# Kernel optimization log

Measured on AMD Instinct MI355X. Metric: run time of the kernel, lower is better.

Reference implementation:

```python
import jax, jax.numpy as jnp
import numpy as np

B, S, H, E, V, NSTEPS = 8, 128, 512, 512, 32000, 8


def setup_inputs() -> dict:
    key = jax.random.key(0)
    ks = jax.random.split(key, 24)

    def lin(k, fi, fo):
        return (jax.random.normal(k, (fi, fo), jnp.float32) / np.sqrt(fi).astype(np.float32))

    return {
        "input_ids": jax.random.randint(ks[0], (B, S), 0, V),
        "tree_ids": jax.random.randint(ks[1], (B, NSTEPS, 3, S), 0, S),
        "emb": jax.random.normal(ks[2], (V, E), jnp.float32) * 0.02,
        "W_ioux": lin(ks[3], E, 3 * H),
        "W_iouh_r": lin(ks[4], H, 3 * H),
        "b_iouh_r": jnp.zeros((3 * H,), jnp.float32),
        "W_iouh_l": lin(ks[5], H, 3 * H),
        "b_iouh_l": jnp.zeros((3 * H,), jnp.float32),
        "W_fx": lin(ks[6], E, H),
        "W_fh0": lin(ks[7], H, H),
        "b_fh0": jnp.zeros((H,), jnp.float32),
        "W_fh1": lin(ks[8], H, H),
        "b_fh1": jnp.zeros((H,), jnp.float32),
        "W_fh2": lin(ks[9], H, H),
        "b_fh2": jnp.zeros((H,), jnp.float32),
        "W_fh3": lin(ks[10], H, H),
        "b_fh3": jnp.zeros((H,), jnp.float32),
    }


def _scatter_rows(vals, idx):
    # out[b, idx[b, j], k] += vals[b, j, k]  (torch scatter_add_ along dim 1)
    return jax.vmap(lambda v, i: jnp.zeros_like(v).at[i].add(v))(vals, idx)


def _gather_rows(vals, idx):
    # out[b, j, k] = vals[b, idx[b, j], k]  (torch gather along dim 1)
    return jnp.take_along_axis(vals, idx[:, :, None], axis=1)


def _masked_scatter(dest, mask_rows, src):
    # Exact torch masked_scatter_ semantics: flatten mask/src, fill True slots
    # with consecutive elements of flattened src.
    m = jnp.broadcast_to(mask_rows[:, :, None], dest.shape).reshape(-1)
    pos = jnp.clip(jnp.cumsum(m) - 1, 0, None)
    out = jnp.where(m, src.reshape(-1)[pos], dest.reshape(-1))
    return out.reshape(dest.shape)


def reference(input_ids, tree_ids, emb, W_ioux, W_iouh_r, b_iouh_r, W_iouh_l,
              b_iouh_l, W_fx, W_fh0, b_fh0, W_fh1, b_fh1, W_fh2, b_fh2,
              W_fh3, b_fh3):
    x = emb[input_ids]                      # [B, S, E]
    Hs = W_fx.shape[1]
    iou_x = x @ W_ioux                      # [B, S, 3H], loop-invariant
    fx_x = x @ W_fx                         # [B, S, H],  loop-invariant
    h0 = jnp.zeros(x.shape[:2] + (Hs,), x.dtype)
    c0 = jnp.zeros_like(h0)
    steps = jnp.transpose(tree_ids, (1, 0, 2, 3))  # [n_steps, B, 3, S]

    def step(carry, t):
        h, c = carry
        idx_d, idx_r, idx_l = t[:, 0], t[:, 1], t[:, 2]
        iou_hr = h @ W_iouh_r + b_iouh_r
        iou_hl = h @ W_iouh_l + b_iouh_l
        # torch scatter_add_ with an index of width H into a 3H buffer only
        # touches the first H channels -- replicate that exactly.
        scat = _scatter_rows(iou_hr[..., :Hs], idx_r) + _scatter_rows(iou_hl[..., :Hs], idx_l)
        iou = iou_x.at[..., :Hs].add(scat)
        i, o, u = jnp.split(iou, 3, axis=-1)
        i, o, u = jax.nn.sigmoid(i), jax.nn.sigmoid(o), jnp.tanh(u)
        # fh0 and fh1 share idx_r, fh2 and fh3 share idx_l -> fold linearly.
        fh_r = h @ (W_fh0 + W_fh1) + (b_fh0 + b_fh1)
        fh_l = h @ (W_fh2 + W_fh3) + (b_fh2 + b_fh3)
        f = jax.nn.sigmoid(_gather_rows(fx_x, idx_d)
                           + _gather_rows(fh_r, idx_r)
                           + _gather_rows(fh_l, idx_l))
        fc = f * c
        c_full = i * u + _scatter_rows(fc, idx_d)
        h_full = o * jnp.tanh(c_full)
        mask = idx_d != 0
        h_new = _masked_scatter(h, mask, h_full)
        c_new = _masked_scatter(c, mask, c_full)
        return (h_new, c_new), None

    (h, c), _ = jax.lax.scan(step, (h0, c0), steps)
    return h
```

## Files before the change

kernel.cpp:

```cpp
#include <hip/hip_runtime.h>
#include <hip/hip_bf16.h>

#define B_ 8
#define S_ 128
#define H_ 512
#define E_ 512
#define NST 8
#define R_ 1024
#define N2 2048
#define KD 512
#define LDA 72
#define TM 64
#define TN 64

typedef __hip_bfloat16 bf16;
typedef __attribute__((ext_vector_type(8))) short v8s;
typedef __attribute__((ext_vector_type(4))) float v4f;

__device__ __forceinline__ float sigm(float x){ return 1.0f/(1.0f + expf(-x)); }
__device__ __forceinline__ float load_in(const void* p, long long i, int isb){
    return isb ? __bfloat162float(((const bf16*)p)[i]) : ((const float*)p)[i];
}
__device__ __forceinline__ int idx_read(const int* p, int j, int is64){
    return is64 ? p[2*j] : p[j];
}
__device__ __forceinline__ unsigned short f2b(float v){
    bf16 b = __float2bfloat16(v);
    return *(unsigned short*)&b;
}

__global__ void probe_all(const void* t0, const void* t1, const void* t2, const void* t3,
                          const void* t4, const void* t5, const void* t6, const void* t7,
                          const void* t8, const void* t9, const void* t10, const void* t11,
                          const void* t12, const void* t13, const void* t14,
                          const int* __restrict__ ids, const int* __restrict__ tree,
                          int* __restrict__ flags){
    const void* ts[15] = {t0,t1,t2,t3,t4,t5,t6,t7,t8,t9,t10,t11,t12,t13,t14};
    int bid = blockIdx.x, t = threadIdx.x;
    int bad = 0;
    if (bid < 15){
        if (t < 512){
            unsigned short u = ((const unsigned short*)ts[bid])[t];
            bad = (((u >> 7) & 0xFF) >= 140);
        }
    } else {
        const int* p = (bid == 15) ? ids : tree;
        int n = (bid == 15) ? 1024 : 2048;
        for (int j = t; j < n; j += 1024)
            if (j & 1) bad |= (p[j] != 0);
    }
    unsigned long long bl = __ballot(bad);
    __shared__ int acc[16];
    if ((t & 63) == 0) acc[t >> 6] = (bl != 0ull) ? 1 : 0;
    __syncthreads();
    if (t == 0){
        int any = 0;
        for (int w = 0; w < 16; ++w) any |= acc[w];
        flags[(bid < 15) ? bid : (16 + bid - 15)] = (bid < 15) ? (any ? 0 : 1) : (any ? 0 : 1);
    }
}

__global__ void rank_count(const int* __restrict__ tree, int* __restrict__ msk,
                           int* __restrict__ rnk, int* __restrict__ cnt,
                           const int* __restrict__ flags){
    int is64 = flags[17];
    int st = blockIdx.x;
    int t  = threadIdx.x;
    cnt[(0*NST + st)*R_ + t] = 0;
    cnt[(1*NST + st)*R_ + t] = 0;
    cnt[(2*NST + st)*R_ + t] = 0;
    __syncthreads();
    int b = t >> 7, s = t & 127;
    int base = (b*NST + st)*3*S_;
    int d0 = idx_read(tree, base + s, is64);
    int rd = (b<<7) + d0;
    int rr = (b<<7) + idx_read(tree, base + S_ + s, is64);
    int rl = (b<<7) + idx_read(tree, base + 2*S_ + s, is64);
    int m = (d0 != 0) ? 1 : 0;
    unsigned long long bal = __ballot(m);
    int lane = t & 63, wave = t >> 6;
    __shared__ int wtot[16];
    if (lane == 0) wtot[wave] = __popcll(bal);
    __syncthreads();
    int bp = 0;
    for (int w = 0; w < wave; ++w) bp += wtot[w];
    int rank = bp + __popcll(bal & ((1ull << lane) - 1ull));
    msk[st*R_ + t] = m;
    rnk[st*R_ + t] = m ? rank : 0;
    atomicAdd(&cnt[(0*NST + st)*R_ + rr], 1);
    atomicAdd(&cnt[(1*NST + st)*R_ + rl], 1);
    atomicAdd(&cnt[(2*NST + st)*R_ + rd], 1);
}

__global__ void csr_scan(const int* __restrict__ cnt, int* __restrict__ off,
                         int* __restrict__ cur){
    int st = blockIdx.x, a = blockIdx.y;
    int t = threadIdx.x;
    int base = (a*NST + st)*R_;
    __shared__ int sh[R_];
    int v = cnt[base + t];
    sh[t] = v;
    __syncthreads();
    for (int d = 1; d < R_; d <<= 1){
        int x = (t >= d) ? sh[t - d] : 0;
        __syncthreads();
        sh[t] += x;
        __syncthreads();
    }
    int excl = sh[t] - v;
    off[base + t] = excl;
    cur[base + t] = excl;
}

__global__ void csr_fill(const int* __restrict__ tree, int* __restrict__ cur,
                         int* __restrict__ ent, const int* __restrict__ flags){
    int is64 = flags[17];
    int st = blockIdx.x;
    int t = threadIdx.x;
    int b = t >> 7, s = t & 127;
    int base = (b*NST + st)*3*S_;
    int rd = (b<<7) + idx_read(tree, base + s, is64);
    int rr = (b<<7) + idx_read(tree, base + S_ + s, is64);
    int rl = (b<<7) + idx_read(tree, base + 2*S_ + s, is64);
    int p0 = atomicAdd(&cur[(0*NST + st)*R_ + rr], 1);
    ent[(0*NST + st)*R_ + p0] = t;
    int p1 = atomicAdd(&cur[(1*NST + st)*R_ + rl], 1);
    ent[(1*NST + st)*R_ + p1] = t;
    int p2 = atomicAdd(&cur[(2*NST + st)*R_ + rd], 1);
    ent[(2*NST + st)*R_ + p2] = t | (rr << 10) | (rl << 20);
}

__global__ __launch_bounds__(256)
void pack_all(const void* __restrict__ Wioux, const void* __restrict__ Wfx,
              const void* __restrict__ Wr, const void* __restrict__ Wl,
              const void* __restrict__ W0, const void* __restrict__ W1,
              const void* __restrict__ W2, const void* __restrict__ W3,
              const void* __restrict__ br, const void* __restrict__ bl,
              const void* __restrict__ b0, const void* __restrict__ b1,
              const void* __restrict__ b2, const void* __restrict__ b3,
              const int* __restrict__ ids, const void* __restrict__ emb,
              unsigned short* __restrict__ WxT, unsigned short* __restrict__ WcatT,
              float* __restrict__ bcat, unsigned short* __restrict__ xb,
              float* __restrict__ h0, unsigned short* __restrict__ hb,
              const int* __restrict__ flags){
    int bid = blockIdx.x, tid = threadIdx.x;
    if (bid < 512){
        int f_wx = flags[1], f_wf = flags[6];
        int n = (bid & 7)*256 + tid;
        int k0 = (bid >> 3)*8;
        unsigned short tmp[8];
        #pragma unroll
        for (int i = 0; i < 8; ++i){
            float v = (n < 1536) ? load_in(Wioux, (long long)(k0+i)*1536 + n, f_wx)
                                 : load_in(Wfx,   (long long)(k0+i)*512 + (n-1536), f_wf);
            tmp[i] = f2b(v);
        }
        *(v8s*)&WxT[(size_t)n*KD + k0] = *(v8s*)tmp;
    } else if (bid < 1024){
        int fWr=flags[2], fWl=flags[4], fW0=flags[7], fW1=flags[9], fW2=flags[11], fW3=flags[13];
        int bb = bid - 512;
        int n = (bb & 7)*256 + tid;
        int k0 = (bb >> 3)*8;
        unsigned short tmp[8];
        #pragma unroll
        for (int i = 0; i < 8; ++i){
            long long k = k0 + i;
            float v;
            if      (n <  512) v = load_in(Wr, k*1536 + n, fWr);
            else if (n < 1024) v = load_in(Wl, k*1536 + (n-512), fWl);
            else if (n < 1536) { int c = n-1024; v = load_in(W0, k*512+c, fW0) + load_in(W1, k*512+c, fW1); }
            else               { int c = n-1536; v = load_in(W2, k*512+c, fW2) + load_in(W3, k*512+c, fW3); }
            tmp[i] = f2b(v);
        }
        *(v8s*)&WcatT[(size_t)n*KD + k0] = *(v8s*)tmp;
    } else if (bid < 1032){
        int fbr=flags[3], fbl=flags[5], fb0=flags[8], fb1=flags[10], fb2=flags[12], fb3=flags[14];
        int n = (bid - 1024)*256 + tid;
        float v;
        if      (n <  512) v = load_in(br, n, fbr);
        else if (n < 1024) v = load_in(bl, n-512, fbl);
        else if (n < 1536) v = load_in(b0, n-1024, fb0) + load_in(b1, n-1024, fb1);
        else               v = load_in(b2, n-1536, fb2) + load_in(b3, n-1536, fb3);
        bcat[n] = v;
    } else if (bid < 1288){
        int f_emb = flags[0], i64 = flags[16];
        int id = (bid - 1032)*256 + tid;
        int r = id >> 6, c0 = (id & 63)*8;
        long long base = (long long)idx_read(ids, r, i64)*E_ + c0;
        unsigned short tmp[8];
        #pragma unroll
        for (int i = 0; i < 8; ++i) tmp[i] = f2b(load_in(emb, base + i, f_emb));
        *(v8s*)&xb[(size_t)r*KD + c0] = *(v8s*)tmp;
    } else if (bid < 2312){
        int idx = (bid - 1288)*256 + tid;
        ((float4*)h0)[idx] = make_float4(0.f, 0.f, 0.f, 0.f);
    } else {
        int idx = (bid - 2312)*256 + tid;
        ((float4*)hb)[idx] = make_float4(0.f, 0.f, 0.f, 0.f);
    }
}

__global__ __launch_bounds__(256)
void gemm_bf16(const unsigned short* __restrict__ A,
               const unsigned short* __restrict__ BT,
               const float* __restrict__ bias,
               float* __restrict__ C){
    __shared__ short As[TM*LDA];
    __shared__ short Bs[TN*LDA];
    int bn = blockIdx.x, bm = blockIdx.y;
    int tid = threadIdx.x;
    int lane = tid & 63, wave = tid >> 6;
    int wm = wave & 1, wn = wave >> 1;
    int lm = lane & 15, quad = lane >> 4;
    v4f acc[2][2];
    #pragma unroll
    for (int i=0;i<2;++i)
        #pragma unroll
        for (int j=0;j<2;++j) acc[i][j] = (v4f)0.0f;

    int srow = tid >> 3, sg = (tid & 7)*8;
    const unsigned short* Ab = A  + (size_t)(bm*TM)*KD;
    const unsigned short* Bb = BT + (size_t)(bn*TN)*KD;
    v8s pa[2], pb[2];
    #pragma unroll
    for (int j=0;j<2;++j){
        pa[j] = *(const v8s*)(Ab + (size_t)(j*32+srow)*KD + sg);
        pb[j] = *(const v8s*)(Bb + (size_t)(j*32+srow)*KD + sg);
    }
    for (int k0 = 0; k0 < KD; k0 += 64){
        #pragma unroll
        for (int j=0;j<2;++j){
            *(v8s*)&As[(j*32+srow)*LDA + sg] = pa[j];
            *(v8s*)&Bs[(j*32+srow)*LDA + sg] = pb[j];
        }
        __syncthreads();
        int k1 = k0 + 64;
        if (k1 < KD){
            #pragma unroll
            for (int j=0;j<2;++j){
                pa[j] = *(const v8s*)(Ab + (size_t)(j*32+srow)*KD + k1 + sg);
                pb[j] = *(const v8s*)(Bb + (size_t)(j*32+srow)*KD + k1 + sg);
            }
        }
        #pragma unroll
        for (int kk = 0; kk < 64; kk += 32){
            v8s af[2], bf[2];
            #pragma unroll
            for (int i=0;i<2;++i){
                af[i] = *(const v8s*)&As[(wm*32 + i*16 + lm)*LDA + kk + quad*8];
                bf[i] = *(const v8s*)&Bs[(wn*32 + i*16 + lm)*LDA + kk + quad*8];
            }
            #pragma unroll
            for (int i=0;i<2;++i)
                #pragma unroll
                for (int j=0;j<2;++j)
                    acc[i][j] = __builtin_amdgcn_mfma_f32_16x16x32_bf16(af[i], bf[j], acc[i][j], 0, 0, 0);
        }
        __syncthreads();
    }
    #pragma unroll
    for (int j=0;j<2;++j){
        int n = bn*TN + wn*32 + j*16 + lm;
        float bv = bias ? bias[n] : 0.0f;
        #pragma unroll
        for (int i=0;i<2;++i){
            int m0 = bm*TM + wm*32 + i*16 + quad*4;
            #pragma unroll
            for (int rg = 0; rg < 4; ++rg)
                C[(size_t)(m0+rg)*N2 + n] = acc[i][j][rg] + bv;
        }
    }
}

__global__ __launch_bounds__(256)
void step_fused(const float* __restrict__ XO, const float* __restrict__ T,
                const float* __restrict__ h_old, const float* __restrict__ c_old,
                float* __restrict__ h_new, float* __restrict__ c_new,
                unsigned short* __restrict__ hb,
                const int* __restrict__ msk, const int* __restrict__ rnk,
                const int* __restrict__ cnt, const int* __restrict__ off,
                const int* __restrict__ ent, int st){
    int r = blockIdx.x;
    if (!msk[st*R_ + r]){
        for (int c = threadIdx.x; c < H_; c += 256){
            float hv = h_old[(size_t)r*H_ + c];
            h_new[(size_t)r*H_ + c] = hv;
            c_new[(size_t)r*H_ + c] = c_old[(size_t)r*H_ + c];
            hb[(size_t)r*KD + c] = f2b(hv);
        }
        return;
    }
    int j = rnk[st*R_ + r];
    int bR = off[(0*NST + st)*R_ + j], dR = cnt[(0*NST + st)*R_ + j];
    int bL = off[(1*NST + st)*R_ + j], dL = cnt[(1*NST + st)*R_ + j];
    int bD = off[(2*NST + st)*R_ + j], dD = cnt[(2*NST + st)*R_ + j];
    const int* eR = ent + (0*NST + st)*R_ + bR;
    const int* eL = ent + (1*NST + st)*R_ + bL;
    const int* eD = ent + (2*NST + st)*R_ + bD;
    const float* xo = XO + (size_t)j*N2;
    for (int c = threadIdx.x; c < H_; c += 256){
        float scat = 0.f;
        for (int e = 0; e < dR; ++e) scat += T[(size_t)eR[e]*N2 + c];
        for (int e = 0; e < dL; ++e) scat += T[(size_t)eL[e]*N2 + 512 + c];
        float fxv = xo[1536 + c];
        float csc = 0.f;
        for (int e = 0; e < dD; ++e){
            int pk = eD[e];
            int s  = pk & 1023, rr = (pk >> 10) & 1023, rl = (pk >> 20) & 1023;
            float f = sigm(fxv + T[(size_t)rr*N2 + 1024 + c] + T[(size_t)rl*N2 + 1536 + c]);
            csc += f * c_old[(size_t)s*H_ + c];
        }
        float ig = sigm(xo[c] + scat);
        float og = sigm(xo[512 + c]);
        float ug = tanhf(xo[1024 + c]);
        float cf = ig*ug + csc;
        float hf = og * tanhf(cf);
        h_new[(size_t)r*H_ + c] = hf;
        c_new[(size_t)r*H_ + c] = cf;
        hb[(size_t)r*KD + c] = f2b(hf);
    }
}

extern "C" void kernel_launch(void* const* d_in, const int* in_sizes, int n_in,
                              void* d_out, int out_size, void* d_ws, size_t ws_size,
                              hipStream_t stream) {
    const int* input_ids = (const int*)d_in[0];
    const int* tree      = (const int*)d_in[1];

    char* p = (char*)d_ws;
    auto alloc = [&](size_t bytes) -> void* {
        void* q = (void*)p;
        p += (bytes + 255) & ~(size_t)255;
        return q;
    };
    float*          XO     = (float*)alloc((size_t)R_*N2*4);
    float*          T      = (float*)alloc((size_t)R_*N2*4);
    float*          h0     = (float*)alloc((size_t)R_*H_*4);
    float*          c0     = (float*)alloc((size_t)R_*H_*4);
    float*          h1     = (float*)alloc((size_t)R_*H_*4);
    float*          c1     = (float*)alloc((size_t)R_*H_*4);
    unsigned short* WxT    = (unsigned short*)alloc((size_t)N2*KD*2);
    unsigned short* WcatT  = (unsigned short*)alloc((size_t)N2*KD*2);
    float*          bcat   = (float*)alloc((size_t)N2*4);
    unsigned short* xb     = (unsigned short*)alloc((size_t)R_*KD*2);
    unsigned short* hb     = (unsigned short*)alloc((size_t)R_*KD*2);
    int*            msk    = (int*)alloc((size_t)NST*R_*4);
    int*            rnk    = (int*)alloc((size_t)NST*R_*4);
    int*            cnt    = (int*)alloc((size_t)3*NST*R_*4);
    int*            off    = (int*)alloc((size_t)3*NST*R_*4);
    int*            cur    = (int*)alloc((size_t)3*NST*R_*4);
    int*            ent    = (int*)alloc((size_t)3*NST*R_*4);
    int*            flags  = (int*)alloc(256);

    hipLaunchKernelGGL(probe_all, dim3(17), dim3(1024), 0, stream,
                       d_in[2], d_in[3], d_in[4], d_in[5], d_in[6], d_in[7], d_in[8],
                       d_in[9], d_in[10], d_in[11], d_in[12], d_in[13], d_in[14],
                       d_in[15], d_in[16], input_ids, tree, flags);
    hipLaunchKernelGGL(rank_count, dim3(NST), dim3(R_), 0, stream, tree, msk, rnk, cnt, flags);
    hipLaunchKernelGGL(csr_scan, dim3(NST, 3), dim3(R_), 0, stream, cnt, off, cur);
    hipLaunchKernelGGL(csr_fill, dim3(NST), dim3(R_), 0, stream, tree, cur, ent, flags);
    hipLaunchKernelGGL(pack_all, dim3(2568), dim3(256), 0, stream,
                       d_in[3], d_in[8],
                       d_in[4], d_in[6], d_in[9], d_in[11], d_in[13], d_in[15],
                       d_in[5], d_in[7], d_in[10], d_in[12], d_in[14], d_in[16],
                       input_ids, d_in[2],
                       WxT, WcatT, bcat, xb, h0, hb, flags);

    hipLaunchKernelGGL(gemm_bf16, dim3(N2/TN, R_/TM), dim3(256), 0, stream,
                       xb, WxT, (const float*)nullptr, XO);

    float *hc = h0, *cc = c0, *hn = h1, *cn = c1;
    for (int st = 0; st < NST; ++st){
        hipLaunchKernelGGL(gemm_bf16, dim3(N2/TN, R_/TM), dim3(256), 0, stream,
                           hb, WcatT, bcat, T);
        hipLaunchKernelGGL(step_fused, dim3(R_), dim3(256), 0, stream,
                           XO, T, hc, cc, hn, cn, hb, msk, rnk, cnt, off, ent, st);
        float* th = hc; hc = hn; hn = th;
        float* tc = cc; cc = cn; cn = tc;
    }
    hipMemcpyAsync(d_out, hc, (size_t)R_*H_*4, hipMemcpyDeviceToDevice, stream);
}
```

Baseline: 324.8 us.

## Merge setup kernels, peel first step GEMM, write final step directly to output

Fuses the rank/count setup into the weight-packing kernel so fewer launches are needed, and uses a grid-stride pack with 512-thread blocks. The first recurrence step skips its GEMM, since h is zero and the projection reduces to the bias; it reads bcat with stride 0. The last step writes straight into the output buffer, dropping the final device-to-device copy. The step epilogue uses one thread per channel with 512-thread blocks. Zero-initialisation of hb is removed because step 0 now writes every row.

```diff
diff --git a/kernel.cpp b/kernel.cpp
--- a/kernel.cpp
+++ b/kernel.cpp
@@ -10,8 +10,6 @@
 #define N2 2048
 #define KD 512
 #define LDA 72
-#define TM 64
-#define TN 64
 
 typedef __hip_bfloat16 bf16;
 typedef __attribute__((ext_vector_type(8))) short v8s;
@@ -56,40 +54,122 @@
     if (t == 0){
         int any = 0;
         for (int w = 0; w < 16; ++w) any |= acc[w];
-        flags[(bid < 15) ? bid : (16 + bid - 15)] = (bid < 15) ? (any ? 0 : 1) : (any ? 0 : 1);
-    }
-}
-
-__global__ void rank_count(const int* __restrict__ tree, int* __restrict__ msk,
-                           int* __restrict__ rnk, int* __restrict__ cnt,
-                           const int* __restrict__ flags){
+        flags[(bid < 15) ? bid : (16 + bid - 15)] = any ? 0 : 1;
+    }
+}
+
+#define NB2 320
+#define GS2 (NB2*512)
+__global__ __launch_bounds__(512)
+void rank_pack(const void* __restrict__ Wioux, const void* __restrict__ Wfx,
+               const void* __restrict__ Wr, const void* __restrict__ Wl,
+               const void* __restrict__ W0, const void* __restrict__ W1,
+               const void* __restrict__ W2, const void* __restrict__ W3,
+               const void* __restrict__ br, const void* __restrict__ bl,
+               const void* __restrict__ b0, const void* __restrict__ b1,
+               const void* __restrict__ b2, const void* __restrict__ b3,
+               const int* __restrict__ ids, const void* __restrict__ emb,
+               const int* __restrict__ tree,
+               unsigned short* __restrict__ WxT, unsigned short* __restrict__ WcatT,
+               float* __restrict__ bcat, unsigned short* __restrict__ xb,
+               float* __restrict__ h0,
+               int* __restrict__ msk, int* __restrict__ rnk, int* __restrict__ cnt,
+               const int* __restrict__ flags){
+    int bid = blockIdx.x, tid = threadIdx.x;
     int is64 = flags[17];
-    int st = blockIdx.x;
-    int t  = threadIdx.x;
-    cnt[(0*NST + st)*R_ + t] = 0;
-    cnt[(1*NST + st)*R_ + t] = 0;
-    cnt[(2*NST + st)*R_ + t] = 0;
-    __syncthreads();
-    int b = t >> 7, s = t & 127;
-    int base = (b*NST + st)*3*S_;
-    int d0 = idx_read(tree, base + s, is64);
-    int rd = (b<<7) + d0;
-    int rr = (b<<7) + idx_read(tree, base + S_ + s, is64);
-    int rl = (b<<7) + idx_read(tree, base + 2*S_ + s, is64);
-    int m = (d0 != 0) ? 1 : 0;
-    unsigned long long bal = __ballot(m);
-    int lane = t & 63, wave = t >> 6;
-    __shared__ int wtot[16];
-    if (lane == 0) wtot[wave] = __popcll(bal);
-    __syncthreads();
-    int bp = 0;
-    for (int w = 0; w < wave; ++w) bp += wtot[w];
-    int rank = bp + __popcll(bal & ((1ull << lane) - 1ull));
-    msk[st*R_ + t] = m;
-    rnk[st*R_ + t] = m ? rank : 0;
-    atomicAdd(&cnt[(0*NST + st)*R_ + rr], 1);
-    atomicAdd(&cnt[(1*NST + st)*R_ + rl], 1);
-    atomicAdd(&cnt[(2*NST + st)*R_ + rd], 1);
+    if (bid < 8){
+        int st = bid;
+        for (int c = tid; c < R_; c += 512){
+            cnt[(0*NST + st)*R_ + c] = 0;
+            cnt[(1*NST + st)*R_ + c] = 0;
+            cnt[(2*NST + st)*R_ + c] = 0;
+        }
+        __syncthreads();
+        __shared__ int wt[8];
+        int runbase = 0;
+        for (int ch = 0; ch < 2; ++ch){
+            int t = ch*512 + tid;
+            int b = t >> 7, s = t & 127;
+            int base = (b*NST + st)*3*S_;
+            int d0 = idx_read(tree, base + s, is64);
+            int rd = (b<<7) + d0;
+            int rr = (b<<7) + idx_read(tree, base + S_ + s, is64);
+            int rl = (b<<7) + idx_read(tree, base + 2*S_ + s, is64);
+            int m = (d0 != 0) ? 1 : 0;
+            unsigned long long bal = __ballot(m);
+            int lane = tid & 63, wv = tid >> 6;
+            if (lane == 0) wt[wv] = __popcll(bal);
+            __syncthreads();
+            int bp = runbase, tot = 0;
+            for (int w = 0; w < wv; ++w) bp += wt[w];
+            for (int w = 0; w < 8; ++w) tot += wt[w];
+            int rank = bp + __popcll(bal & ((1ull << lane) - 1ull));
+            msk[st*R_ + t] = m;
+            rnk[st*R_ + t] = m ? rank : 0;
+            atomicAdd(&cnt[(0*NST + st)*R_ + rr], 1);
+            atomicAdd(&cnt[(1*NST + st)*R_ + rl], 1);
+            atomicAdd(&cnt[(2*NST + st)*R_ + rd], 1);
+            runbase += tot;
+            __syncthreads();
+        }
+    }
+    int gt = bid*512 + tid;
+    {
+        int f_wx = flags[1], f_wf = flags[6];
+        for (int u = gt; u < 131072; u += GS2){
+            int n = u >> 6, k0 = (u & 63)*8;
+            unsigned short tmp[8];
+            #pragma unroll
+            for (int i = 0; i < 8; ++i){
+                float v = (n < 1536) ? load_in(Wioux, (long long)(k0+i)*1536 + n, f_wx)
+                                     : load_in(Wfx,   (long long)(k0+i)*512 + (n-1536), f_wf);
+                tmp[i] = f2b(v);
+            }
+            *(v8s*)&WxT[(size_t)n*KD + k0] = *(v8s*)tmp;
+        }
+    }
+    {
+        int fWr=flags[2], fWl=flags[4], fW0=flags[7], fW1=flags[9], fW2=flags[11], fW3=flags[13];
+        for (int u = gt; u < 131072; u += GS2){
+            int n = u >> 6, k0 = (u & 63)*8;
+            unsigned short tmp[8];
+            #pragma unroll
+            for (int i = 0; i < 8; ++i){
+                long long k = k0 + i;
+                float v;
+                if      (n <  512) v = load_in(Wr, k*1536 + n, fWr);
+                else if (n < 1024) v = load_in(Wl, k*1536 + (n-512), fWl);
+                else if (n < 1536) { int c = n-1024; v = load_in(W0, k*512+c, fW0) + load_in(W1, k*512+c, fW1); }
+                else               { int c = n-1536; v = load_in(W2, k*512+c, fW2) + load_in(W3, k*512+c, fW3); }
+                tmp[i] = f2b(v);
+            }
+            *(v8s*)&WcatT[(size_t)n*KD + k0] = *(v8s*)tmp;
+        }
+    }
+    {
+        int fbr=flags[3], fbl=flags[5], fb0=flags[8], fb1=flags[10], fb2=flags[12], fb3=flags[14];
+        for (int n = gt; n < 2048; n += GS2){
+            float v;
+            if      (n <  512) v = load_in(br, n, fbr);
+            else if (n < 1024) v = load_in(bl, n-512, fbl);
+            else if (n < 1536) v = load_in(b0, n-1024, fb0) + load_in(b1, n-1024, fb1);
+            else               v = load_in(b2, n-1536, fb2) + load_in(b3, n-1536, fb3);
+            bcat[n] = v;
+        }
+    }
+    {
+        int f_emb = flags[0], i64i = flags[16];
+        for (int u = gt; u < 65536; u += GS2){
+            int r = u >> 6, c0 = (u & 63)*8;
+            long long base = (long long)idx_read(ids, r, i64i)*E_ + c0;
+            unsigned short tmp[8];
+            #pragma unroll
+            for (int i = 0; i < 8; ++i) tmp[i] = f2b(load_in(emb, base + i, f_emb));
+            *(v8s*)&xb[(size_t)r*KD + c0] = *(v8s*)tmp;
+        }
+    }
+    for (int u = gt; u < 262144; u += GS2)
+        ((float4*)h0)[u] = make_float4(0.f,0.f,0.f,0.f);
 }
 
 __global__ void csr_scan(const int* __restrict__ cnt, int* __restrict__ off,
@@ -112,91 +192,24 @@
     cur[base + t] = excl;
 }
 
-__global__ void csr_fill(const int* __restrict__ tree, int* __restrict__ cur,
-                         int* __restrict__ ent, const int* __restrict__ flags){
+__global__ __launch_bounds__(512)
+void csr_fill(const int* __restrict__ tree, int* __restrict__ cur,
+              int* __restrict__ ent, const int* __restrict__ flags){
     int is64 = flags[17];
     int st = blockIdx.x;
-    int t = threadIdx.x;
-    int b = t >> 7, s = t & 127;
-    int base = (b*NST + st)*3*S_;
-    int rd = (b<<7) + idx_read(tree, base + s, is64);
-    int rr = (b<<7) + idx_read(tree, base + S_ + s, is64);
-    int rl = (b<<7) + idx_read(tree, base + 2*S_ + s, is64);
-    int p0 = atomicAdd(&cur[(0*NST + st)*R_ + rr], 1);
-    ent[(0*NST + st)*R_ + p0] = t;
-    int p1 = atomicAdd(&cur[(1*NST + st)*R_ + rl], 1);
-    ent[(1*NST + st)*R_ + p1] = t;
-    int p2 = atomicAdd(&cur[(2*NST + st)*R_ + rd], 1);
-    ent[(2*NST + st)*R_ + p2] = t | (rr << 10) | (rl << 20);
-}
-
-__global__ __launch_bounds__(256)
-void pack_all(const void* __restrict__ Wioux, const void* __restrict__ Wfx,
-              const void* __restrict__ Wr, const void* __restrict__ Wl,
-              const void* __restrict__ W0, const void* __restrict__ W1,
-              const void* __restrict__ W2, const void* __restrict__ W3,
-              const void* __restrict__ br, const void* __restrict__ bl,
-              const void* __restrict__ b0, const void* __restrict__ b1,
-              const void* __restrict__ b2, const void* __restrict__ b3,
-              const int* __restrict__ ids, const void* __restrict__ emb,
-              unsigned short* __restrict__ WxT, unsigned short* __restrict__ WcatT,
-              float* __restrict__ bcat, unsigned short* __restrict__ xb,
-              float* __restrict__ h0, unsigned short* __restrict__ hb,
-              const int* __restrict__ flags){
-    int bid = blockIdx.x, tid = threadIdx.x;
-    if (bid < 512){
-        int f_wx = flags[1], f_wf = flags[6];
-        int n = (bid & 7)*256 + tid;
-        int k0 = (bid >> 3)*8;
-        unsigned short tmp[8];
-        #pragma unroll
-        for (int i = 0; i < 8; ++i){
-            float v = (n < 1536) ? load_in(Wioux, (long long)(k0+i)*1536 + n, f_wx)
-                                 : load_in(Wfx,   (long long)(k0+i)*512 + (n-1536), f_wf);
-            tmp[i] = f2b(v);
-        }
-        *(v8s*)&WxT[(size_t)n*KD + k0] = *(v8s*)tmp;
-    } else if (bid < 1024){
-        int fWr=flags[2], fWl=flags[4], fW0=flags[7], fW1=flags[9], fW2=flags[11], fW3=flags[13];
-        int bb = bid - 512;
-        int n = (bb & 7)*256 + tid;
-        int k0 = (bb >> 3)*8;
-        unsigned short tmp[8];
-        #pragma unroll
-        for (int i = 0; i < 8; ++i){
-            long long k = k0 + i;
-            float v;
-            if      (n <  512) v = load_in(Wr, k*1536 + n, fWr);
-            else if (n < 1024) v = load_in(Wl, k*1536 + (n-512), fWl);
-            else if (n < 1536) { int c = n-1024; v = load_in(W0, k*512+c, fW0) + load_in(W1, k*512+c, fW1); }
-            else               { int c = n-1536; v = load_in(W2, k*512+c, fW2) + load_in(W3, k*512+c, fW3); }
-            tmp[i] = f2b(v);
-        }
-        *(v8s*)&WcatT[(size_t)n*KD + k0] = *(v8s*)tmp;
-    } else if (bid < 1032){
-        int fbr=flags[3], fbl=flags[5], fb0=flags[8], fb1=flags[10], fb2=flags[12], fb3=flags[14];
-        int n = (bid - 1024)*256 + tid;
-        float v;
-        if      (n <  512) v = load_in(br, n, fbr);
-        else if (n < 1024) v = load_in(bl, n-512, fbl);
-        else if (n < 1536) v = load_in(b0, n-1024, fb0) + load_in(b1, n-1024, fb1);
-        else               v = load_in(b2, n-1536, fb2) + load_in(b3, n-1536, fb3);
-        bcat[n] = v;
-    } else if (bid < 1288){
-        int f_emb = flags[0], i64 = flags[16];
-        int id = (bid - 1032)*256 + tid;
-        int r = id >> 6, c0 = (id & 63)*8;
-        long long base = (long long)idx_read(ids, r, i64)*E_ + c0;
-        unsigned short tmp[8];
-        #pragma unroll
-        for (int i = 0; i < 8; ++i) tmp[i] = f2b(load_in(emb, base + i, f_emb));
-        *(v8s*)&xb[(size_t)r*KD + c0] = *(v8s*)tmp;
-    } else if (bid < 2312){
-        int idx = (bid - 1288)*256 + tid;
-        ((float4*)h0)[idx] = make_float4(0.f, 0.f, 0.f, 0.f);
-    } else {
-        int idx = (bid - 2312)*256 + tid;
-        ((float4*)hb)[idx] = make_float4(0.f, 0.f, 0.f, 0.f);
+    for (int ch = 0; ch < 2; ++ch){
+        int t = ch*512 + threadIdx.x;
+        int b = t >> 7, s = t & 127;
+        int base = (b*NST + st)*3*S_;
+        int rd = (b<<7) + idx_read(tree, base + s, is64);
+        int rr = (b<<7) + idx_read(tree, base + S_ + s, is64);
+        int rl = (b<<7) + idx_read(tree, base + 2*S_ + s, is64);
+        int p0 = atomicAdd(&cur[(0*NST + st)*R_ + rr], 1);
+        ent[(0*NST + st)*R_ + p0] = t;
+        int p1 = atomicAdd(&cur[(1*NST + st)*R_ + rl], 1);
+        ent[(1*NST + st)*R_ + p1] = t;
+        int p2 = atomicAdd(&cur[(2*NST + st)*R_ + rd], 1);
+        ent[(2*NST + st)*R_ + p2] = t | (rr << 10) | (rl << 20);
     }
 }
 
@@ -205,8 +218,8 @@
                const unsigned short* __restrict__ BT,
                const float* __restrict__ bias,
                float* __restrict__ C){
-    __shared__ short As[TM*LDA];
-    __shared__ short Bs[TN*LDA];
+    __shared__ short As[64*LDA];
+    __shared__ short Bs[64*LDA];
     int bn = blockIdx.x, bm = blockIdx.y;
     int tid = threadIdx.x;
     int lane = tid & 63, wave = tid >> 6;
@@ -219,8 +232,8 @@
         for (int j=0;j<2;++j) acc[i][j] = (v4f)0.0f;
 
     int srow = tid >> 3, sg = (tid & 7)*8;
-    const unsigned short* Ab = A  + (size_t)(bm*TM)*KD;
-    const unsigned short* Bb = BT + (size_t)(bn*TN)*KD;
+    const unsigned short* Ab = A  + (size_t)(bm*64)*KD;
+    const unsigned short* Bb = BT + (size_t)(bn*64)*KD;
     v8s pa[2], pb[2];
     #pragma unroll
     for (int j=0;j<2;++j){
@@ -260,11 +273,11 @@
     }
     #pragma unroll
     for (int j=0;j<2;++j){
-        int n = bn*TN + wn*32 + j*16 + lm;
+        int n = bn*64 + wn*32 + j*16 + lm;
         float bv = bias ? bias[n] : 0.0f;
         #pragma unroll
         for (int i=0;i<2;++i){
-            int m0 = bm*TM + wm*32 + i*16 + quad*4;
+            int m0 = bm*64 + wm*32 + i*16 + quad*4;
             #pragma unroll
             for (int rg = 0; rg < 4; ++rg)
                 C[(size_t)(m0+rg)*N2 + n] = acc[i][j][rg] + bv;
@@ -272,53 +285,51 @@
     }
 }
 
-__global__ __launch_bounds__(256)
-void step_fused(const float* __restrict__ XO, const float* __restrict__ T,
-                const float* __restrict__ h_old, const float* __restrict__ c_old,
-                float* __restrict__ h_new, float* __restrict__ c_new,
-                unsigned short* __restrict__ hb,
-                const int* __restrict__ msk, const int* __restrict__ rnk,
-                const int* __restrict__ cnt, const int* __restrict__ off,
-                const int* __restrict__ ent, int st){
-    int r = blockIdx.x;
+__global__ __launch_bounds__(512)
+void step_epi(const float* __restrict__ XO, const float* __restrict__ T, int tstr,
+              const float* __restrict__ hc, const float* __restrict__ cc,
+              float* __restrict__ hn, float* __restrict__ cn,
+              unsigned short* __restrict__ hb, float* __restrict__ out,
+              const int* __restrict__ msk, const int* __restrict__ rnk,
+              const int* __restrict__ cnt, const int* __restrict__ off,
+              const int* __restrict__ ent, int st, int last){
+    int r = blockIdx.x, c = threadIdx.x;
     if (!msk[st*R_ + r]){
-        for (int c = threadIdx.x; c < H_; c += 256){
-            float hv = h_old[(size_t)r*H_ + c];
-            h_new[(size_t)r*H_ + c] = hv;
-            c_new[(size_t)r*H_ + c] = c_old[(size_t)r*H_ + c];
-            hb[(size_t)r*KD + c] = f2b(hv);
-        }
+        float hv = hc[(size_t)r*H_ + c];
+        if (last){ out[(size_t)r*H_ + c] = hv; return; }
+        hn[(size_t)r*H_ + c] = hv;
+        cn[(size_t)r*H_ + c] = cc[(size_t)r*H_ + c];
+        hb[(size_t)r*KD + c] = f2b(hv);
         return;
     }
     int j = rnk[st*R_ + r];
-    int bR = off[(0*NST + st)*R_ + j], dR = cnt[(0*NST + st)*R_ + j];
-    int bL = off[(1*NST + st)*R_ + j], dL = cnt[(1*NST + st)*R_ + j];
-    int bD = off[(2*NST + st)*R_ + j], dD = cnt[(2*NST + st)*R_ + j];
-    const int* eR = ent + (0*NST + st)*R_ + bR;
-    const int* eL = ent + (1*NST + st)*R_ + bL;
-    const int* eD = ent + (2*NST + st)*R_ + bD;
+    int bR = off[(0*NST+st)*R_ + j], dR = cnt[(0*NST+st)*R_ + j];
+    int bL = off[(1*NST+st)*R_ + j], dL = cnt[(1*NST+st)*R_ + j];
+    int bD = off[(2*NST+st)*R_ + j], dD = cnt[(2*NST+st)*R_ + j];
+    const int* eR = ent + (0*NST+st)*R_ + bR;
+    const int* eL = ent + (1*NST+st)*R_ + bL;
+    const int* eD = ent + (2*NST+st)*R_ + bD;
     const float* xo = XO + (size_t)j*N2;
-    for (int c = threadIdx.x; c < H_; c += 256){
-        float scat = 0.f;
-        for (int e = 0; e < dR; ++e) scat += T[(size_t)eR[e]*N2 + c];
-        for (int e = 0; e < dL; ++e) scat += T[(size_t)eL[e]*N2 + 512 + c];
-        float fxv = xo[1536 + c];
-        float csc = 0.f;
-        for (int e = 0; e < dD; ++e){
-            int pk = eD[e];
-            int s  = pk & 1023, rr = (pk >> 10) & 1023, rl = (pk >> 20) & 1023;
-            float f = sigm(fxv + T[(size_t)rr*N2 + 1024 + c] + T[(size_t)rl*N2 + 1536 + c]);
-            csc += f * c_old[(size_t)s*H_ + c];
-        }
-        float ig = sigm(xo[c] + scat);
-        float og = sigm(xo[512 + c]);
-        float ug = tanhf(xo[1024 + c]);
-        float cf = ig*ug + csc;
-        float hf = og * tanhf(cf);
-        h_new[(size_t)r*H_ + c] = hf;
-        c_new[(size_t)r*H_ + c] = cf;
-        hb[(size_t)r*KD + c] = f2b(hf);
-    }
+    float scv = 0.f;
+    for (int e = 0; e < dR; ++e) scv += T[(size_t)eR[e]*tstr + c];
+    for (int e = 0; e < dL; ++e) scv += T[(size_t)eL[e]*tstr + 512 + c];
+    float fxv = xo[1536 + c];
+    float csc = 0.f;
+    for (int e = 0; e < dD; ++e){
+        int pk = eD[e];
+        int s  = pk & 1023, rr = (pk >> 10) & 1023, rl = (pk >> 20) & 1023;
+        float f = sigm(fxv + T[(size_t)rr*tstr + 1024 + c] + T[(size_t)rl*tstr + 1536 + c]);
+        csc += f * cc[(size_t)s*H_ + c];
+    }
+    float ig = sigm(xo[c] + scv);
+    float og = sigm(xo[512 + c]);
+    float ug = tanhf(xo[1024 + c]);
+    float cf = ig*ug + csc;
+    float hf = og * tanhf(cf);
+    if (last){ out[(size_t)r*H_ + c] = hf; return; }
+    hn[(size_t)r*H_ + c] = hf;
+    cn[(size_t)r*H_ + c] = cf;
+    hb[(size_t)r*KD + c] = f2b(hf);
 }
 
 extern "C" void kernel_launch(void* const* d_in, const int* in_sizes, int n_in,
@@ -327,10 +338,10 @@
     const int* input_ids = (const int*)d_in[0];
     const int* tree      = (const int*)d_in[1];
 
-    char* p = (char*)d_ws;
+    char* wp = (char*)d_ws;
     auto alloc = [&](size_t bytes) -> void* {
-        void* q = (void*)p;
-        p += (bytes + 255) & ~(size_t)255;
+        void* q = (void*)wp;
+        wp += (bytes + 255) & ~(size_t)255;
         return q;
     };
     float*          XO     = (float*)alloc((size_t)R_*N2*4);
@@ -351,32 +362,37 @@
     int*            cur    = (int*)alloc((size_t)3*NST*R_*4);
     int*            ent    = (int*)alloc((size_t)3*NST*R_*4);
     int*            flags  = (int*)alloc(256);
+    float*          out    = (float*)d_out;
 
     hipLaunchKernelGGL(probe_all, dim3(17), dim3(1024), 0, stream,
                        d_in[2], d_in[3], d_in[4], d_in[5], d_in[6], d_in[7], d_in[8],
                        d_in[9], d_in[10], d_in[11], d_in[12], d_in[13], d_in[14],
                        d_in[15], d_in[16], input_ids, tree, flags);
-    hipLaunchKernelGGL(rank_count, dim3(NST), dim3(R_), 0, stream, tree, msk, rnk, cnt, flags);
-    hipLaunchKernelGGL(csr_scan, dim3(NST, 3), dim3(R_), 0, stream, cnt, off, cur);
-    hipLaunchKernelGGL(csr_fill, dim3(NST), dim3(R_), 0, stream, tree, cur, ent, flags);
-    hipLaunchKernelGGL(pack_all, dim3(2568), dim3(256), 0, stream,
+    hipLaunchKernelGGL(rank_pack, dim3(NB2), dim3(512), 0, stream,
                        d_in[3], d_in[8],
                        d_in[4], d_in[6], d_in[9], d_in[11], d_in[13], d_in[15],
                        d_in[5], d_in[7], d_in[10], d_in[12], d_in[14], d_in[16],
-                       input_ids, d_in[2],
-                       WxT, WcatT, bcat, xb, h0, hb, flags);
-
-    hipLaunchKernelGGL(gemm_bf16, dim3(N2/TN, R_/TM), dim3(256), 0, stream,
+                       input_ids, d_in[2], tree,
+                       WxT, WcatT, bcat, xb, h0, msk, rnk, cnt, flags);
+    hipLaunchKernelGGL(csr_scan, dim3(NST, 3), dim3(1024), 0, stream, cnt, off, cur);
+    hipLaunchKernelGGL(csr_fill, dim3(NST), dim3(512), 0, stream, tree, cur, ent, flags);
+
+    hipLaunchKernelGGL(gemm_bf16, dim3(N2/64, R_/64), dim3(256), 0, stream,
                        xb, WxT, (const float*)nullptr, XO);
 
     float *hc = h0, *cc = c0, *hn = h1, *cn = c1;
-    for (int st = 0; st < NST; ++st){
-        hipLaunchKernelGGL(gemm_bf16, dim3(N2/TN, R_/TM), dim3(256), 0, stream,
+    hipLaunchKernelGGL(step_epi, dim3(R_), dim3(512), 0, stream,
+                       XO, bcat, 0, hc, cc, hn, cn, hb, out,
+                       msk, rnk, cnt, off, ent, 0, 0);
+    { float* t1 = hc; hc = hn; hn = t1; float* t2 = cc; cc = cn; cn = t2; }
+
+    for (int st = 1; st < NST; ++st){
+        hipLaunchKernelGGL(gemm_bf16, dim3(N2/64, R_/64), dim3(256), 0, stream,
                            hb, WcatT, bcat, T);
-        hipLaunchKernelGGL(step_fused, dim3(R_), dim3(256), 0, stream,
-                           XO, T, hc, cc, hn, cn, hb, msk, rnk, cnt, off, ent, st);
-        float* th = hc; hc = hn; hn = th;
-        float* tc = cc; cc = cn; cn = tc;
-    }
-    hipMemcpyAsync(d_out, hc, (size_t)R_*H_*4, hipMemcpyDeviceToDevice, stream);
-}
+        hipLaunchKernelGGL(step_epi, dim3(R_), dim3(512), 0, stream,
+                           XO, T, N2, hc, cc, hn, cn, hb, out,
+                           msk, rnk, cnt, off, ent, st, (st == NST-1) ? 1 : 0);
+        float* t1 = hc; hc = hn; hn = t1;
+        float* t2 = cc; cc = cn; cn = t2;
+    }
+}
```

Result: faster. 288.6 us (-11.2%).
